# Performance work log

Hardware: AMD Instinct MI355X
Metric: run time of the kernel (lower is better)

## Reference

```python
import jax, jax.numpy as jnp
import numpy as np

BS, N, D = 8, 2048, 512


def setup_inputs() -> dict:
    key = jax.random.key(0)
    ks = jax.random.split(key, 8)
    s = 0.05  # small scale keeps exp(k + bias) numerically tame
    inp = jax.random.normal(ks[0], (BS, N, D), dtype=jnp.float32)
    Wq = jax.random.normal(ks[1], (D, D), dtype=jnp.float32) * s
    bq = jax.random.normal(ks[2], (D,), dtype=jnp.float32) * s
    Wk = jax.random.normal(ks[3], (D, D), dtype=jnp.float32) * s
    bk = jax.random.normal(ks[4], (D,), dtype=jnp.float32) * s
    Wv = jax.random.normal(ks[5], (D, D), dtype=jnp.float32) * s
    bv = jax.random.normal(ks[6], (D,), dtype=jnp.float32) * s
    pos_bias = jax.random.normal(ks[7], (N, N), dtype=jnp.float32) * s
    return {"input": inp, "Wq": Wq, "bq": bq, "Wk": Wk, "bk": bk,
            "Wv": Wv, "bv": bv, "pos_bias": pos_bias}


def reference(input, Wq, bq, Wk, bk, Wv, bv, pos_bias):
    # q, k, v projections: (bs, n, d)
    q = input @ Wq + bq
    k = input @ Wk + bk
    v = input @ Wv + bv
    # AFT-Full: out[b,i,d] = sigmoid(q)[b,i,d] *
    #   sum_j exp(k[b,j,d] + B[i,j]) * v[b,j,d] / sum_j exp(k[b,j,d] + B[i,j])
    # Factor exp(k + B) = exp(B) * exp(k): avoids the (n,bs,n,d) broadcast,
    # identical math to the torch source.
    ek = jnp.exp(k)                       # (bs, n, d)
    eB = jnp.exp(pos_bias)                # (n, n), rows = query pos i
    numerator = jnp.einsum('ij,bjd->bid', eB, ek * v)
    denominator = jnp.einsum('ij,bjd->bid', eB, ek)
    return jax.nn.sigmoid(q) * (numerator / denominator)
```

## Files before the change

### kernel.cpp

```cpp
#include <hip/hip_runtime.h>
#include <stdint.h>

#define N_SEQ 2048
#define D_MODEL 512
#define MROWS 16384
#define XCOLS 8192

typedef __attribute__((ext_vector_type(8))) short bf16x8;
typedef __attribute__((ext_vector_type(4))) float f32x4;

__device__ __forceinline__ short f2bf(float f) {
  union { float f; uint32_t u; } x; x.f = f;
  uint32_t r = x.u + 0x7FFFu + ((x.u >> 16) & 1u);
  return (short)(uint16_t)(r >> 16);
}
__device__ __forceinline__ unsigned short f2h(float f) {
  union { _Float16 h; unsigned short u; } x; x.h = (_Float16)f; return x.u;
}
__device__ __forceinline__ float h2f(unsigned short u) {
  union { unsigned short u; _Float16 h; } x; x.u = u; return (float)x.h;
}

__device__ __forceinline__ void gload_lds16(const void* g, void* l) {
  __builtin_amdgcn_global_load_lds(
      (__attribute__((address_space(1))) void*)(void*)g,
      (__attribute__((address_space(3))) void*)l, 16, 0, 0);
}


__global__ void k_conv_bf16(const float* __restrict__ in,
                            short* __restrict__ a, int n4) {
  int stride = gridDim.x * blockDim.x;
  for (int i = blockIdx.x * blockDim.x + threadIdx.x; i < n4; i += stride) {
    float4 v = reinterpret_cast<const float4*>(in)[i];
    short4 h;
    h.x = f2bf(v.x); h.y = f2bf(v.y); h.z = f2bf(v.z); h.w = f2bf(v.w);
    reinterpret_cast<short4*>(a)[i] = h;
  }
}

__global__ void k_prep_eb(const float* __restrict__ pb, short* __restrict__ eb,
                          int n4) {
  int stride = gridDim.x * blockDim.x;
  for (int i = blockIdx.x * blockDim.x + threadIdx.x; i < n4; i += stride) {
    float4 v = reinterpret_cast<const float4*>(pb)[i];
    short4 o;
    o.x = f2bf(expf(v.x));
    o.y = f2bf(expf(v.y));
    o.z = f2bf(expf(v.z));
    o.w = f2bf(expf(v.w));
    reinterpret_cast<short4*>(eb)[i] = o;
  }
}

__global__ void k_prep_w(const float* __restrict__ Wq, const float* __restrict__ Wk,
                         const float* __restrict__ Wv, short* __restrict__ wh) {
  int t = blockIdx.x * blockDim.x + threadIdx.x;
  if (t >= 1536 * 512) return;
  int c = t >> 9, k = t & 511;
  float v;
  if (c < 512) v = Wq[k * 512 + c];
  else {
    int cc = c - 512, d = cc >> 1;
    v = (cc & 1) ? Wv[k * 512 + d] : Wk[k * 512 + d];
  }
  wh[t] = f2bf(v);
}

__global__ __launch_bounds__(256) void k_proj(
    const short* __restrict__ A, const short* __restrict__ W,
    const float* __restrict__ bq, const float* __restrict__ bk,
    const float* __restrict__ bv,
    unsigned short* __restrict__ sigq, short* __restrict__ Xt) {
  __shared__ short lA[128 * 64], lB[128 * 64];
  const int tid = threadIdx.x;
  const int lane = tid & 63, wid = tid >> 6;
  const int wr = wid >> 1, wc = wid & 1;
  const int lrow = lane & 15;
  const int kq = (lane >> 4) << 4;
  const int row0 = blockIdx.x * 128;
  const int col0 = blockIdx.y * 128;

  const f32x4 fzero = {0.f, 0.f, 0.f, 0.f};
  f32x4 acc[4][4];
#pragma unroll
  for (int m = 0; m < 4; ++m)
#pragma unroll
    for (int n = 0; n < 4; ++n) acc[m][n] = fzero;

  const short* gA = A + row0 * 512;
  const short* gB = W + col0 * 512;

  for (int kt = 0; kt < 8; ++kt) {
    const int kb = kt * 64;
#pragma unroll
    for (int p = 0; p < 4; ++p) {
      int c = p * 256 + tid;
      int B = c << 4;
      int r = B >> 7;
      int wp = (B & 127) ^ ((r & 7) << 4);
      int ke = wp >> 1;
      int goff = r * 512 + kb + ke;
      int loff = (p * 256 + wid * 64) << 3;
      gload_lds16(gA + goff, lA + loff);
      gload_lds16(gB + goff, lB + loff);
    }
    __syncthreads();
#pragma unroll
    for (int ks = 0; ks < 2; ++ks) {
      int kb2 = kq + ks * 64;
      bf16x8 fb[4];
#pragma unroll
      for (int n = 0; n < 4; ++n) {
        int r = wc * 64 + n * 16 + lrow;
        fb[n] = *(const bf16x8*)((const char*)lB + (r << 7) +
                                 (kb2 ^ ((r & 7) << 4)));
      }
#pragma unroll
      for (int m = 0; m < 4; ++m) {
        int r = wr * 64 + m * 16 + lrow;
        bf16x8 fa = *(const bf16x8*)((const char*)lA + (r << 7) +
                                     (kb2 ^ ((r & 7) << 4)));
#pragma unroll
        for (int n = 0; n < 4; ++n)
          acc[m][n] = __builtin_amdgcn_mfma_f32_16x16x32_bf16(fa, fb[n], acc[m][n], 0, 0, 0);
      }
    }
    __syncthreads();
  }

  const int rbase = row0 + wr * 64 + ((lane >> 4) << 2);
  if (col0 < 512) {
#pragma unroll
    for (int n = 0; n < 4; ++n) {
      int c = col0 + wc * 64 + n * 16 + lrow;
      float bias = bq[c];
#pragma unroll
      for (int m = 0; m < 4; ++m) {
        int gr = rbase + m * 16;
#pragma unroll
        for (int r = 0; r < 4; ++r) {
          float q = acc[m][n][r] + bias;
          sigq[(gr + r) * 512 + c] = f2h(1.f / (1.f + expf(-q)));
        }
      }
    }
  } else {
    int s = lane & 1;
#pragma unroll
    for (int n = 0; n < 4; ++n) {
      int c = col0 + wc * 64 + n * 16 + lrow;
      int d = (c - 512) >> 1;
      float bias = s ? bv[d] : bk[d];
#pragma unroll
      for (int m = 0; m < 4; ++m) {
        int gr = rbase + m * 16;
        int b = gr >> 11;
        int j = gr & 2047;
        f32x4 val;
#pragma unroll
        for (int r = 0; r < 4; ++r) val[r] = acc[m][n][r] + bias;
        if (!s) {
#pragma unroll
          for (int r = 0; r < 4; ++r) val[r] = expf(val[r]);
        }
        f32x4 oth;
#pragma unroll
        for (int r = 0; r < 4; ++r) oth[r] = __shfl_xor(val[r], 1);
        if (!s) {
          short4 wq, eq;
          wq.x = f2bf(val[0] * oth[0]); eq.x = f2bf(val[0]);
          wq.y = f2bf(val[1] * oth[1]); eq.y = f2bf(val[1]);
          wq.z = f2bf(val[2] * oth[2]); eq.z = f2bf(val[2]);
          wq.w = f2bf(val[3] * oth[3]); eq.w = f2bf(val[3]);
          int colp = b * 1024 + 2 * d;
          *(short4*)&Xt[colp * 2048 + j] = wq;
          *(short4*)&Xt[(colp + 1) * 2048 + j] = eq;
        }
      }
    }
  }
}

__global__ __launch_bounds__(256) void k_main(
    const short* __restrict__ eB, const short* __restrict__ Xt,
    const unsigned short* __restrict__ sigq, float* __restrict__ out) {
  __shared__ short lA[128 * 64], lB[128 * 64];
  const int tid = threadIdx.x;
  const int lane = tid & 63, wid = tid >> 6;
  const int wr = wid >> 1, wc = wid & 1;
  const int lrow = lane & 15;
  const int kq = (lane >> 4) << 4;
  const int row0 = blockIdx.x * 128;
  const int col0 = blockIdx.y * 128;

  const f32x4 fzero = {0.f, 0.f, 0.f, 0.f};
  f32x4 acc[4][4];
#pragma unroll
  for (int m = 0; m < 4; ++m)
#pragma unroll
    for (int n = 0; n < 4; ++n) acc[m][n] = fzero;

  const short* gA = eB + row0 * 2048;
  const short* gB = Xt + col0 * 2048;

  for (int kt = 0; kt < 32; ++kt) {
    const int kb = kt * 64;
#pragma unroll
    for (int p = 0; p < 4; ++p) {
      int c = p * 256 + tid;
      int B = c << 4;
      int r = B >> 7;
      int wp = (B & 127) ^ ((r & 7) << 4);
      int ke = wp >> 1;
      int goff = r * 2048 + kb + ke;
      int loff = (p * 256 + wid * 64) << 3;
      gload_lds16(gA + goff, lA + loff);
      gload_lds16(gB + goff, lB + loff);
    }
    __syncthreads();
#pragma unroll
    for (int ks = 0; ks < 2; ++ks) {
      int kb2 = kq + ks * 64;
      bf16x8 fb[4];
#pragma unroll
      for (int n = 0; n < 4; ++n) {
        int r = wc * 64 + n * 16 + lrow;
        fb[n] = *(const bf16x8*)((const char*)lB + (r << 7) +
                                 (kb2 ^ ((r & 7) << 4)));
      }
#pragma unroll
      for (int m = 0; m < 4; ++m) {
        int r = wr * 64 + m * 16 + lrow;
        bf16x8 fa = *(const bf16x8*)((const char*)lA + (r << 7) +
                                     (kb2 ^ ((r & 7) << 4)));
#pragma unroll
        for (int n = 0; n < 4; ++n)
          acc[m][n] = __builtin_amdgcn_mfma_f32_16x16x32_bf16(fa, fb[n], acc[m][n], 0, 0, 0);
      }
    }
    __syncthreads();
  }

  const int rbase = row0 + wr * 64 + ((lane >> 4) << 2);
#pragma unroll
  for (int n = 0; n < 4; ++n) {
    int c = col0 + wc * 64 + n * 16 + lrow;
    int b = c >> 10;
    int d = (c & 1023) >> 1;
#pragma unroll
    for (int m = 0; m < 4; ++m) {
      f32x4 den;
#pragma unroll
      for (int r = 0; r < 4; ++r) den[r] = __shfl_xor(acc[m][n][r], 1);
      if ((lane & 1) == 0) {
#pragma unroll
        for (int r = 0; r < 4; ++r) {
          int i = rbase + m * 16 + r;
          int idx = (b * 2048 + i) * 512 + d;
          float sg = h2f(sigq[idx]);
          out[idx] = sg * (acc[m][n][r] / den[r]);
        }
      }
    }
  }
}

extern "C" void kernel_launch(void* const* d_in, const int* in_sizes, int n_in,
                              void* d_out, int out_size, void* d_ws, size_t ws_size,
                              hipStream_t stream) {
  const float* in = (const float*)d_in[0];
  const float* Wq = (const float*)d_in[1];
  const float* bq = (const float*)d_in[2];
  const float* Wk = (const float*)d_in[3];
  const float* bk = (const float*)d_in[4];
  const float* Wv = (const float*)d_in[5];
  const float* bv = (const float*)d_in[6];
  const float* pb = (const float*)d_in[7];
  float* out = (float*)d_out;

  char* ws = (char*)d_ws;
  short* Xt = (short*)ws;
  short* eB = (short*)(ws + 33554432);
  short* Ah = (short*)(ws + 41943040);
  short* Wh = (short*)(ws + 58720256);
  unsigned short* sigq = (unsigned short*)(ws + 60293120);

  k_conv_bf16<<<2048, 256, 0, stream>>>(in, Ah, MROWS * D_MODEL / 4);
  k_prep_w<<<3072, 256, 0, stream>>>(Wq, Wk, Wv, Wh);
  k_prep_eb<<<2048, 256, 0, stream>>>(pb, eB, N_SEQ * N_SEQ / 4);

  dim3 gp(128, 12);
  k_proj<<<gp, 256, 0, stream>>>(Ah, Wh, bq, bk, bv, sigq, Xt);

  dim3 gm(16, 64);
  k_main<<<gm, 256, 0, stream>>>(eB, Xt, sigq, out);
}
```

Baseline: 164.4 us.

## Rewrite main GEMM as 256x256 tile, 8-wave, double-buffered ping-pong pipeline

Replaces the 128x128 four-wave main GEMM kernel with a 256x256 tile computed by 8 waves, using 128 KB of dynamic LDS split into two buffers. Global-to-LDS loads for the next k-tiles are interleaved between MFMA phases, with explicit vmcnt waits, barriers and setprio scheduling. The aim is to hide memory latency and raise data reuse per tile. In exchange it runs one block per CU, uses fewer blocks (256), and needs careful barrier and wait counting for correctness.

New measurement: 148.8 us. -9.5%, faster.

```diff
diff --git a/kernel.cpp b/kernel.cpp
--- a/kernel.cpp
+++ b/kernel.cpp
@@ -4,7 +4,7 @@
 #define N_SEQ 2048
 #define D_MODEL 512
 #define MROWS 16384
-#define XCOLS 8192
+#define NT_K 32
 
 typedef __attribute__((ext_vector_type(8))) short bf16x8;
 typedef __attribute__((ext_vector_type(4))) float f32x4;
@@ -182,84 +182,158 @@
   }
 }
 
-__global__ __launch_bounds__(256) void k_main(
+
+#define MM(FA, FB, NH)                                                      \
+  {                                                                         \
+    _Pragma("unroll") for (int mm_ = 0; mm_ < 8; ++mm_) {                   \
+      acc[mm_][2 * (NH)] = __builtin_amdgcn_mfma_f32_16x16x32_bf16(         \
+          FA[mm_], FB[2 * (NH)], acc[mm_][2 * (NH)], 0, 0, 0);              \
+      acc[mm_][2 * (NH) + 1] = __builtin_amdgcn_mfma_f32_16x16x32_bf16(     \
+          FA[mm_], FB[2 * (NH) + 1], acc[mm_][2 * (NH) + 1], 0, 0, 0);      \
+    }                                                                       \
+  }
+
+#define PHASE_MID()                                     \
+  __builtin_amdgcn_sched_barrier(0);                    \
+  __builtin_amdgcn_s_barrier();                         \
+  asm volatile("s_waitcnt lgkmcnt(0)" ::: "memory");    \
+  __builtin_amdgcn_sched_barrier(0);                    \
+  __builtin_amdgcn_s_setprio(1)
+
+#define PHASE_END()                                     \
+  __builtin_amdgcn_s_setprio(0);                        \
+  __builtin_amdgcn_sched_barrier(0);                    \
+  __builtin_amdgcn_s_barrier()
+
+#define VMCNT4() asm volatile("s_waitcnt vmcnt(4)" ::: "memory")
+
+__global__ __launch_bounds__(512, 1) void k_main8(
     const short* __restrict__ eB, const short* __restrict__ Xt,
     const unsigned short* __restrict__ sigq, float* __restrict__ out) {
-  __shared__ short lA[128 * 64], lB[128 * 64];
+  extern __shared__ short lds[];
   const int tid = threadIdx.x;
   const int lane = tid & 63, wid = tid >> 6;
-  const int wr = wid >> 1, wc = wid & 1;
+  const int wr = wid >> 2, wc = wid & 3;
   const int lrow = lane & 15;
-  const int kq = (lane >> 4) << 4;
-  const int row0 = blockIdx.x * 128;
-  const int col0 = blockIdx.y * 128;
+  const int khi = (lane >> 4) << 4;
+  const int row0 = blockIdx.x * 256;
+  const int col0 = blockIdx.y * 256;
 
   const f32x4 fzero = {0.f, 0.f, 0.f, 0.f};
-  f32x4 acc[4][4];
-#pragma unroll
-  for (int m = 0; m < 4; ++m)
+  f32x4 acc[8][4];
+#pragma unroll
+  for (int m = 0; m < 8; ++m)
 #pragma unroll
     for (int n = 0; n < 4; ++n) acc[m][n] = fzero;
 
   const short* gA = eB + row0 * 2048;
   const short* gB = Xt + col0 * 2048;
 
-  for (int kt = 0; kt < 32; ++kt) {
-    const int kb = kt * 64;
-#pragma unroll
-    for (int p = 0; p < 4; ++p) {
-      int c = p * 256 + tid;
-      int B = c << 4;
-      int r = B >> 7;
-      int wp = (B & 127) ^ ((r & 7) << 4);
-      int ke = wp >> 1;
-      int goff = r * 2048 + kb + ke;
-      int loff = (p * 256 + wid * 64) << 3;
-      gload_lds16(gA + goff, lA + loff);
-      gload_lds16(gB + goff, lB + loff);
-    }
-    __syncthreads();
-#pragma unroll
-    for (int ks = 0; ks < 2; ++ks) {
-      int kb2 = kq + ks * 64;
-      bf16x8 fb[4];
-#pragma unroll
-      for (int n = 0; n < 4; ++n) {
-        int r = wc * 64 + n * 16 + lrow;
-        fb[n] = *(const bf16x8*)((const char*)lB + (r << 7) +
-                                 (kb2 ^ ((r & 7) << 4)));
-      }
-#pragma unroll
-      for (int m = 0; m < 4; ++m) {
-        int r = wr * 64 + m * 16 + lrow;
-        bf16x8 fa = *(const bf16x8*)((const char*)lA + (r << 7) +
-                                     (kb2 ^ ((r & 7) << 4)));
-#pragma unroll
-        for (int n = 0; n < 4; ++n)
-          acc[m][n] = __builtin_amdgcn_mfma_f32_16x16x32_bf16(fa, fb[n], acc[m][n], 0, 0, 0);
-      }
-    }
-    __syncthreads();
-  }
-
-  const int rbase = row0 + wr * 64 + ((lane >> 4) << 2);
+  auto STAGE = [&](int kt, int isB, int h) {
+    int ktc = kt < NT_K ? kt : NT_K - 1;
+    const short* src = (isB ? gB : gA) + (h * 128) * 2048 + ktc * 64;
+    int sbase = ((ktc & 1) << 15) + (isB << 14) + (h << 13);
+#pragma unroll
+    for (int p = 0; p < 2; ++p) {
+      int c = p * 512 + tid;
+      int r = c >> 3;
+      int ke = ((((c & 7) << 4) ^ ((r & 7) << 4)) >> 1);
+      gload_lds16(src + r * 2048 + ke,
+                  lds + sbase + ((p * 512 + wid * 64) << 3));
+    }
+  };
+  auto LDA = [&](int buf, int ks, int m) -> bf16x8 {
+    int R = wr * 128 + m * 16 + lrow;
+    int kb = ks * 64 + khi;
+    return *(const bf16x8*)((const char*)lds + (buf << 16) + R * 128 +
+                            (kb ^ ((R & 7) << 4)));
+  };
+  auto LDB = [&](int buf, int ks, int n) -> bf16x8 {
+    int Rc = wc * 64 + n * 16 + lrow;
+    int kb = ks * 64 + khi;
+    return *(const bf16x8*)((const char*)lds + (buf << 16) + 32768 +
+                            Rc * 128 + (kb ^ ((Rc & 7) << 4)));
+  };
+
+  STAGE(0, 0, 0); STAGE(0, 0, 1); STAGE(0, 1, 0); STAGE(0, 1, 1);
+  STAGE(1, 0, 0); STAGE(1, 0, 1);
+  VMCNT4();
+  __builtin_amdgcn_sched_barrier(0);
+  __builtin_amdgcn_s_barrier();
+
+  bf16x8 fa0[8], fa1[8], fb0[4], fb1[4];
+
+  for (int it = 0; it < NT_K / 2; ++it) {
+    const int t0 = 2 * it, t1 = 2 * it + 1;
+#pragma unroll
+    for (int m = 0; m < 8; ++m) fa0[m] = LDA(0, 0, m);
+#pragma unroll
+    for (int n = 0; n < 4; ++n) fb0[n] = LDB(0, 0, n);
+    STAGE(t1, 1, 0);
+    PHASE_MID();
+    MM(fa0, fb0, 0);
+    PHASE_END();
+#pragma unroll
+    for (int m = 0; m < 8; ++m) fa1[m] = LDA(0, 1, m);
+#pragma unroll
+    for (int n = 0; n < 4; ++n) fb1[n] = LDB(0, 1, n);
+    STAGE(t1, 1, 1);
+    PHASE_MID();
+    MM(fa0, fb0, 1);
+    PHASE_END();
+    STAGE(t0 + 2, 0, 0);
+    PHASE_MID();
+    MM(fa1, fb1, 0);
+    PHASE_END();
+    STAGE(t0 + 2, 0, 1);
+    VMCNT4();
+    PHASE_MID();
+    MM(fa1, fb1, 1);
+    PHASE_END();
+#pragma unroll
+    for (int m = 0; m < 8; ++m) fa0[m] = LDA(1, 0, m);
+#pragma unroll
+    for (int n = 0; n < 4; ++n) fb0[n] = LDB(1, 0, n);
+    STAGE(t0 + 2, 1, 0);
+    PHASE_MID();
+    MM(fa0, fb0, 0);
+    PHASE_END();
+#pragma unroll
+    for (int m = 0; m < 8; ++m) fa1[m] = LDA(1, 1, m);
+#pragma unroll
+    for (int n = 0; n < 4; ++n) fb1[n] = LDB(1, 1, n);
+    STAGE(t0 + 2, 1, 1);
+    PHASE_MID();
+    MM(fa0, fb0, 1);
+    PHASE_END();
+    STAGE(t1 + 2, 0, 0);
+    PHASE_MID();
+    MM(fa1, fb1, 0);
+    PHASE_END();
+    STAGE(t1 + 2, 0, 1);
+    VMCNT4();
+    PHASE_MID();
+    MM(fa1, fb1, 1);
+    PHASE_END();
+  }
+
+  const int rbase = row0 + wr * 128 + ((lane >> 4) << 2);
 #pragma unroll
   for (int n = 0; n < 4; ++n) {
     int c = col0 + wc * 64 + n * 16 + lrow;
     int b = c >> 10;
     int d = (c & 1023) >> 1;
 #pragma unroll
-    for (int m = 0; m < 4; ++m) {
+    for (int m = 0; m < 8; ++m) {
       f32x4 den;
 #pragma unroll
       for (int r = 0; r < 4; ++r) den[r] = __shfl_xor(acc[m][n][r], 1);
       if ((lane & 1) == 0) {
 #pragma unroll
         for (int r = 0; r < 4; ++r) {
-          int i = rbase + m * 16 + r;
-          int idx = (b * 2048 + i) * 512 + d;
-          float sg = h2f(sigq[idx]);
-          out[idx] = sg * (acc[m][n][r] / den[r]);
+          int i2 = rbase + m * 16 + r;
+          int idx = (b * 2048 + i2) * 512 + d;
+          out[idx] = h2f(sigq[idx]) * (acc[m][n][r] / den[r]);
         }
       }
     }
@@ -286,6 +360,9 @@
   short* Wh = (short*)(ws + 58720256);
   unsigned short* sigq = (unsigned short*)(ws + 60293120);
 
+  (void)hipFuncSetAttribute((const void*)k_main8,
+                            hipFuncAttributeMaxDynamicSharedMemorySize, 131072);
+
   k_conv_bf16<<<2048, 256, 0, stream>>>(in, Ah, MROWS * D_MODEL / 4);
   k_prep_w<<<3072, 256, 0, stream>>>(Wq, Wk, Wv, Wh);
   k_prep_eb<<<2048, 256, 0, stream>>>(pb, eB, N_SEQ * N_SEQ / 4);
@@ -293,6 +370,6 @@
   dim3 gp(128, 12);
   k_proj<<<gp, 256, 0, stream>>>(Ah, Wh, bq, bk, bv, sigq, Xt);
 
-  dim3 gm(16, 64);
-  k_main<<<gm, 256, 0, stream>>>(eB, Xt, sigq, out);
-}
+  dim3 gm(8, 32);
+  k_main8<<<gm, 512, 131072, stream>>>(eB, Xt, sigq, out);
+}
```

## Use 256x256 tiles with fragment-packed X loaded directly into registers

Applied to the files above, without the earlier changes.

The projection kernel now writes the value/exp tensor in an MFMA-fragment-packed layout, so the main GEMM can load B fragments straight from global memory into registers without staging them in LDS. The main kernel uses 1024-thread blocks computing 256x256 tiles, double-buffers only the eB operand in dynamic LDS, and maps blocks so each XCD shares column tiles. The aim is to cut LDS traffic and synchronisation and to improve L2 reuse. In exchange, B fragments come from uncoalesced-per-block global reads, and the large blocks carry high register pressure.

Result: faster. 150.2 us (-8.6%).

```diff
diff --git a/kernel.cpp b/kernel.cpp
--- a/kernel.cpp
+++ b/kernel.cpp
@@ -4,7 +4,7 @@
 #define N_SEQ 2048
 #define D_MODEL 512
 #define MROWS 16384
-#define XCOLS 8192
+#define NT_K 32
 
 typedef __attribute__((ext_vector_type(8))) short bf16x8;
 typedef __attribute__((ext_vector_type(4))) float f32x4;
@@ -71,7 +71,7 @@
     const short* __restrict__ A, const short* __restrict__ W,
     const float* __restrict__ bq, const float* __restrict__ bk,
     const float* __restrict__ bv,
-    unsigned short* __restrict__ sigq, short* __restrict__ Xt) {
+    unsigned short* __restrict__ sigq, short* __restrict__ Xf) {
   __shared__ short lA[128 * 64], lB[128 * 64];
   const int tid = threadIdx.x;
   const int lane = tid & 63, wid = tid >> 6;
@@ -174,25 +174,34 @@
           wq.z = f2bf(val[2] * oth[2]); eq.z = f2bf(val[2]);
           wq.w = f2bf(val[3] * oth[3]); eq.w = f2bf(val[3]);
           int colp = b * 1024 + 2 * d;
-          *(short4*)&Xt[colp * 2048 + j] = wq;
-          *(short4*)&Xt[(colp + 1) * 2048 + j] = eq;
+          int kg = j >> 5;
+          int sub = ((j >> 3) & 3) << 4;
+          int e0 = j & 4;
+          int ctn = colp >> 4;
+          int lnn = (colp & 15) | sub;
+          int lnd = ((colp + 1) & 15) | sub;
+          *(short4*)&Xf[(((ctn * 64 + kg) * 64 + lnn) << 3) + e0] = wq;
+          *(short4*)&Xf[(((ctn * 64 + kg) * 64 + lnd) << 3) + e0] = eq;
         }
       }
     }
   }
 }
 
-__global__ __launch_bounds__(256) void k_main(
-    const short* __restrict__ eB, const short* __restrict__ Xt,
+__global__ __launch_bounds__(1024, 4) void k_main3(
+    const short* __restrict__ eB, const short* __restrict__ Xf,
     const unsigned short* __restrict__ sigq, float* __restrict__ out) {
-  __shared__ short lA[128 * 64], lB[128 * 64];
+  extern __shared__ short lds[];
   const int tid = threadIdx.x;
   const int lane = tid & 63, wid = tid >> 6;
-  const int wr = wid >> 1, wc = wid & 1;
+  const int wr = wid >> 2, wc = wid & 3;
   const int lrow = lane & 15;
-  const int kq = (lane >> 4) << 4;
-  const int row0 = blockIdx.x * 128;
-  const int col0 = blockIdx.y * 128;
+  const int khi = (lane >> 4) << 4;
+
+  const int bid = blockIdx.x;
+  const int xcd = bid & 7, bj = bid >> 3;
+  const int row0 = (bj & 7) * 256;
+  const int col0 = ((xcd << 2) + (bj >> 3)) * 256;
 
   const f32x4 fzero = {0.f, 0.f, 0.f, 0.f};
   f32x4 acc[4][4];
@@ -202,42 +211,50 @@
     for (int n = 0; n < 4; ++n) acc[m][n] = fzero;
 
   const short* gA = eB + row0 * 2048;
-  const short* gB = Xt + col0 * 2048;
-
-  for (int kt = 0; kt < 32; ++kt) {
-    const int kb = kt * 64;
-#pragma unroll
-    for (int p = 0; p < 4; ++p) {
-      int c = p * 256 + tid;
-      int B = c << 4;
-      int r = B >> 7;
-      int wp = (B & 127) ^ ((r & 7) << 4);
-      int ke = wp >> 1;
-      int goff = r * 2048 + kb + ke;
-      int loff = (p * 256 + wid * 64) << 3;
-      gload_lds16(gA + goff, lA + loff);
-      gload_lds16(gB + goff, lB + loff);
-    }
-    __syncthreads();
+  const int ctbase = (col0 >> 4) + wc * 4;
+
+  auto STAGE = [&](int kt) {
+    const short* src = gA + kt * 64;
+    const int sb = (kt & 1) << 14;
+#pragma unroll
+    for (int p = 0; p < 2; ++p) {
+      int c = p * 1024 + tid;
+      int r = c >> 3;
+      int ke = ((((c & 7) << 4) ^ ((r & 7) << 4)) >> 1);
+      gload_lds16(src + r * 2048 + ke,
+                  lds + sb + ((p * 1024 + wid * 64) << 3));
+    }
+  };
+  auto LDA = [&](int b, int ks, int m) -> bf16x8 {
+    int R = wr * 64 + m * 16 + lrow;
+    int kb = ks * 64 + khi;
+    return *(const bf16x8*)((const char*)lds + (b << 15) + R * 128 +
+                            (kb ^ ((R & 7) << 4)));
+  };
+  auto LDBg = [&](int kt, int ks, int n) -> bf16x8 {
+    int ct = ctbase + n;
+    int kg = kt * 2 + ks;
+    return *(const bf16x8*)(Xf + ((((ct << 6) + kg) << 6) + lane) * 8);
+  };
+
+  STAGE(0);
+  __syncthreads();
+
+  for (int t = 0; t < NT_K; ++t) {
+    const int b = t & 1;
+    if (t + 1 < NT_K) STAGE(t + 1);
 #pragma unroll
     for (int ks = 0; ks < 2; ++ks) {
-      int kb2 = kq + ks * 64;
-      bf16x8 fb[4];
-#pragma unroll
-      for (int n = 0; n < 4; ++n) {
-        int r = wc * 64 + n * 16 + lrow;
-        fb[n] = *(const bf16x8*)((const char*)lB + (r << 7) +
-                                 (kb2 ^ ((r & 7) << 4)));
-      }
-#pragma unroll
-      for (int m = 0; m < 4; ++m) {
-        int r = wr * 64 + m * 16 + lrow;
-        bf16x8 fa = *(const bf16x8*)((const char*)lA + (r << 7) +
-                                     (kb2 ^ ((r & 7) << 4)));
+      bf16x8 fb[4], fa[4];
+#pragma unroll
+      for (int n = 0; n < 4; ++n) fb[n] = LDBg(t, ks, n);
+#pragma unroll
+      for (int m = 0; m < 4; ++m) fa[m] = LDA(b, ks, m);
+#pragma unroll
+      for (int m = 0; m < 4; ++m)
 #pragma unroll
         for (int n = 0; n < 4; ++n)
-          acc[m][n] = __builtin_amdgcn_mfma_f32_16x16x32_bf16(fa, fb[n], acc[m][n], 0, 0, 0);
-      }
+          acc[m][n] = __builtin_amdgcn_mfma_f32_16x16x32_bf16(fa[m], fb[n], acc[m][n], 0, 0, 0);
     }
     __syncthreads();
   }
@@ -256,10 +273,9 @@
       if ((lane & 1) == 0) {
 #pragma unroll
         for (int r = 0; r < 4; ++r) {
-          int i = rbase + m * 16 + r;
-          int idx = (b * 2048 + i) * 512 + d;
-          float sg = h2f(sigq[idx]);
-          out[idx] = sg * (acc[m][n][r] / den[r]);
+          int i2 = rbase + m * 16 + r;
+          int idx = (b * 2048 + i2) * 512 + d;
+          out[idx] = h2f(sigq[idx]) * (acc[m][n][r] / den[r]);
         }
       }
     }
@@ -280,19 +296,21 @@
   float* out = (float*)d_out;
 
   char* ws = (char*)d_ws;
-  short* Xt = (short*)ws;
+  short* Xf = (short*)ws;
   short* eB = (short*)(ws + 33554432);
   short* Ah = (short*)(ws + 41943040);
   short* Wh = (short*)(ws + 58720256);
   unsigned short* sigq = (unsigned short*)(ws + 60293120);
 
+  (void)hipFuncSetAttribute((const void*)k_main3,
+                            hipFuncAttributeMaxDynamicSharedMemorySize, 65536);
+
   k_conv_bf16<<<2048, 256, 0, stream>>>(in, Ah, MROWS * D_MODEL / 4);
   k_prep_w<<<3072, 256, 0, stream>>>(Wq, Wk, Wv, Wh);
   k_prep_eb<<<2048, 256, 0, stream>>>(pb, eB, N_SEQ * N_SEQ / 4);
 
   dim3 gp(128, 12);
-  k_proj<<<gp, 256, 0, stream>>>(Ah, Wh, bq, bk, bv, sigq, Xt);
-
-  dim3 gm(16, 64);
-  k_main<<<gm, 256, 0, stream>>>(eB, Xt, sigq, out);
-}
+  k_proj<<<gp, 256, 0, stream>>>(Ah, Wh, bq, bk, bv, sigq, Xf);
+
+  k_main3<<<dim3(256), 1024, 65536, stream>>>(eB, Xf, sigq, out);
+}
```
